# Kernel tuning notes

Hardware: AMD Instinct MI355X
Metric: run time of the kernel (lower is better)

Reference implementation:

```python
import jax, jax.numpy as jnp
import numpy as np

B, T, F = 4096, 512, 17
H = 32          # hidden_dim
P = 8           # num_prototypes
DEMO = 4
OUT = 1
FP = F + 1      # features + static row
LN_EPS = 1e-5
COS_EPS = 1e-8


def setup_inputs() -> dict:
    key = jax.random.key(0)
    ks = jax.random.split(key, 20)
    s = lambda i, shape, scale=0.1: jax.random.normal(ks[i], shape, jnp.float32) * scale
    return {
        "x": jax.random.normal(ks[0], (B, T, F), jnp.float32),
        "static": jax.random.normal(ks[1], (B, DEMO), jnp.float32),
        # 17 per-feature GRUs (input_size=1), batched along leading F axis
        "W_ih": s(2, (F, 3 * H)),      # squeezed from [F,3H,1]
        "W_hh": s(3, (F, 3 * H, H)),
        "b_ih": s(4, (F, 3 * H)),
        "b_hh": s(5, (F, 3 * H)),
        "demo_W": s(6, (H, DEMO)),
        "demo_b": s(7, (H,)),
        "ln_w": jnp.ones((FP, H), jnp.float32),
        "ln_b": jnp.zeros((FP, H), jnp.float32),
        "prototypes": jax.random.uniform(ks[8], (P, FP, H), jnp.float32),
        "Wq": s(9, (H, P)), "bq": s(10, (H,)),
        "Wk": s(11, (P, FP)), "bk": s(12, (P,)),
        "Wv": s(13, (P, FP)), "bv": s(14, (P,)),
        "out_W": s(15, (OUT, H)), "out_b": s(16, (OUT,)),
    }


def _batched_gru(x, W_ih, W_hh, b_ih, b_hh):
    # x: [B,T,F] -> run F independent GRUs (input dim 1) in parallel. Returns [B,F,H].
    h0 = jnp.zeros((x.shape[0], F, H), x.dtype)

    def step(h, x_t):  # x_t: [B,F]
        ih = x_t[:, :, None] * W_ih[None] + b_ih[None]                 # [B,F,3H]
        hh = jnp.einsum('bfh,fgh->bfg', h, W_hh) + b_hh[None]          # [B,F,3H]
        r = jax.nn.sigmoid(ih[..., :H] + hh[..., :H])
        z = jax.nn.sigmoid(ih[..., H:2 * H] + hh[..., H:2 * H])
        n = jnp.tanh(ih[..., 2 * H:] + r * hh[..., 2 * H:])
        h_new = (1.0 - z) * n + z * h
        return h_new, None

    h_final, _ = jax.lax.scan(step, h0, jnp.transpose(x, (1, 0, 2)))
    return h_final  # [B,F,H]


def reference(x, static, W_ih, W_hh, b_ih, b_hh, demo_W, demo_b,
              ln_w, ln_b, prototypes, Wq, bq, Wk, bk, Wv, bv, out_W, out_b):
    h_t = _batched_gru(x, W_ih, W_hh, b_ih, b_hh)                      # [B,F,H]
    demo = (static @ demo_W.T + demo_b)[:, None, :]                    # [B,1,H]
    h_t = jnp.concatenate([h_t, demo], axis=1)                         # [B,FP,H]
    # LayerNorm over last two dims (FP,H)
    mu = jnp.mean(h_t, axis=(-2, -1), keepdims=True)
    var = jnp.var(h_t, axis=(-2, -1), keepdims=True)
    h_t = (h_t - mu) * jax.lax.rsqrt(var + LN_EPS) * ln_w + ln_b
    # cosine similarity to flattened prototypes -> [B,P]
    hf = h_t.reshape(h_t.shape[0], -1)                                 # [B,FP*H]
    pf = prototypes.reshape(P, -1)                                     # [P,FP*H]
    num = hf @ pf.T
    denom = jnp.maximum(jnp.linalg.norm(hf, axis=-1)[:, None] *
                        jnp.linalg.norm(pf, axis=-1)[None, :], COS_EPS)
    distance = num / denom                                             # [B,P]
    # Attention1 (dropout inactive at eval)
    q = distance @ Wq.T + bq                                           # [B,H]
    input_k = jnp.einsum('bfh,pf->bph', h_t, Wk) + bk[None, :, None]   # [B,P,H]
    input_v = jnp.einsum('bfh,pf->bph', h_t, Wv) + bv[None, :, None]   # [B,P,H]
    e = jnp.einsum('bph,bh->bp', input_k, q)                           # [B,P]
    a = jax.nn.softmax(e, axis=1)
    v = jnp.einsum('bp,bph->bh', a, input_v)                           # [B,H]
    logits = jax.nn.sigmoid(v @ out_W.T + out_b)                       # [B,1]
    return logits, distance, h_t
```

## Files before the change

### kernel.cpp

```cpp
#include <hip/hip_runtime.h>
#include <cmath>

#define Bsz  4096
#define Tlen 512
#define Fnum 17
#define Hdim 32
#define Pnum 8
#define FPn  18
#define G3   96

#define L2E   1.4426950408889634f
#define NL2E (-1.4426950408889634f)
#define TL2E  2.8853900817779268f

typedef __attribute__((ext_vector_type(8))) short short8v;
typedef __attribute__((ext_vector_type(4))) float float4v;

__device__ __forceinline__ float frcp(float x)  { return __builtin_amdgcn_rcpf(x); }
__device__ __forceinline__ float frsq(float x)  { return __builtin_amdgcn_rsqf(x); }
__device__ __forceinline__ float fexp2(float x) { return __builtin_amdgcn_exp2f(x); }
__device__ __forceinline__ float fsigmoid(float x) {
    return frcp(1.0f + fexp2(NL2E * x));
}
__device__ __forceinline__ short bf16b(float x) {
    unsigned u = __float_as_uint(x);
    unsigned r = (u + 0x7FFFu + ((u >> 16) & 1u)) >> 16;
    return (short)r;
}
__device__ __forceinline__ unsigned cvtpk(float lo, float hi) {
    unsigned r;
    asm("v_cvt_pk_bf16_f32 %0, %1, %2" : "=v"(r) : "v"(lo), "v"(hi));
    return r;
}

__global__ void prep_pnorm_kernel(const float* __restrict__ protos, float* __restrict__ pnorm) {
    const int p    = threadIdx.x >> 5;
    const int lane = threadIdx.x & 31;
    float s = 0.0f;
    for (int j = lane; j < FPn * Hdim; j += 32) {
        float v = protos[p * FPn * Hdim + j];
        s = fmaf(v, v, s);
    }
    #pragma unroll
    for (int m = 16; m; m >>= 1) s += __shfl_xor(s, m);
    if (lane == 0) pnorm[p] = sqrtf(s);
}

__global__ __launch_bounds__(64)
void xpose_kernel(const float* __restrict__ x, unsigned short* __restrict__ xT) {
    const int b = blockIdx.x * 64 + threadIdx.x;
    const int t = blockIdx.y;
    const float* __restrict__ xp = x + ((size_t)b * Tlen + t) * Fnum;
    #pragma unroll
    for (int ff = 0; ff < Fnum; ++ff)
        xT[(size_t)ff * (Tlen + 1) * Bsz + (size_t)t * Bsz + b] = (unsigned short)bf16b(xp[ff]);
}

template<int USE_XT>
__global__ __launch_bounds__(256, 4)
void gru_mfma_kernel(const float* __restrict__ x,
                     const unsigned short* __restrict__ xT,
                     const float* __restrict__ Wih,
                     const float* __restrict__ Whh,
                     const float* __restrict__ bih,
                     const float* __restrict__ bhh,
                     float* __restrict__ pre)
{
    const int f  = blockIdx.y;
    const int wv = threadIdx.x >> 6;
    const int l  = threadIdx.x & 63;
    const int B0 = blockIdx.x * 64 + wv * 16;
    const int c  = l & 15, S = l >> 4;
    const int b  = B0 + c;

    const float* __restrict__ whh_f = Whh + (size_t)f * G3 * Hdim;
    const float* __restrict__ wih_f = Wih + (size_t)f * G3;
    const float* __restrict__ bih_f = bih + (size_t)f * G3;
    const float* __restrict__ bhh_f = bhh + (size_t)f * G3;

    short8v afrag0, afrag1, afrag2, afrag3, afrag4, afrag5;
    float4v cinit0, cinit1, cinit2, cinit3, cinit4, cinit5;
    {
        union { short8v s; unsigned u[4]; } au;
        #pragma unroll
        for (int m = 0; m < 6; ++m) {
            const int gate = m >> 1;
            const float sc = (gate < 2) ? NL2E : TL2E;
            const int gA = gate * 32 + 8 * (c >> 2) + (m & 1) * 4 + (c & 3);
            const float* wrow = whh_f + (size_t)gA * Hdim + 8 * S;
            #pragma unroll
            for (int u = 0; u < 4; ++u)
                au.u[u] = cvtpk(wrow[2 * u] * sc, wrow[2 * u + 1] * sc);
            float4v ci;
            #pragma unroll
            for (int q = 0; q < 4; ++q) {
                const int gC = gate * 32 + 8 * S + (m & 1) * 4 + q;
                ci[q] = (gate < 2) ? NL2E * (bhh_f[gC] + bih_f[gC])
                                   : TL2E * bhh_f[gC];
            }
            if (m == 0) { afrag0 = au.s; cinit0 = ci; }
            if (m == 1) { afrag1 = au.s; cinit1 = ci; }
            if (m == 2) { afrag2 = au.s; cinit2 = ci; }
            if (m == 3) { afrag3 = au.s; cinit3 = ci; }
            if (m == 4) { afrag4 = au.s; cinit4 = ci; }
            if (m == 5) { afrag5 = au.s; cinit5 = ci; }
        }
    }
    float wr[8], wz[8], wn[8], bn[8];
    #pragma unroll
    for (int i = 0; i < 8; ++i) {
        const int j = 8 * S + i;
        wr[i] = NL2E * wih_f[j];
        wz[i] = NL2E * wih_f[32 + j];
        wn[i] = TL2E * wih_f[64 + j];
        bn[i] = TL2E * bih_f[64 + j];
    }

    float h[8];
    #pragma unroll
    for (int i = 0; i < 8; ++i) h[i] = 0.0f;

    const unsigned short* xtp = nullptr;
    const float* xp = nullptr;
    float xv_next;
    if (USE_XT) {
        xtp = xT + (size_t)f * (Tlen + 1) * Bsz + b;
        xv_next = __uint_as_float(((unsigned)*xtp) << 16);
    } else {
        xp = x + (size_t)b * Tlen * Fnum + f;
        xv_next = *xp;
    }

    for (int t = 0; t < Tlen; ++t) {
        const float xv = xv_next;
        if (USE_XT) {
            xtp += Bsz;
            xv_next = __uint_as_float(((unsigned)*xtp) << 16);
        } else {
            xp += (t < Tlen - 1) ? Fnum : 0;
            xv_next = *xp;
        }

        union { short8v s; unsigned u[4]; } bu;
        bu.u[0] = cvtpk(h[0], h[1]);
        bu.u[1] = cvtpk(h[2], h[3]);
        bu.u[2] = cvtpk(h[4], h[5]);
        bu.u[3] = cvtpk(h[6], h[7]);

        const float4v a0 = __builtin_amdgcn_mfma_f32_16x16x32_bf16(afrag0, bu.s, cinit0, 0, 0, 0);
        const float4v a1 = __builtin_amdgcn_mfma_f32_16x16x32_bf16(afrag1, bu.s, cinit1, 0, 0, 0);
        const float4v a2 = __builtin_amdgcn_mfma_f32_16x16x32_bf16(afrag2, bu.s, cinit2, 0, 0, 0);
        const float4v a3 = __builtin_amdgcn_mfma_f32_16x16x32_bf16(afrag3, bu.s, cinit3, 0, 0, 0);
        const float4v a4 = __builtin_amdgcn_mfma_f32_16x16x32_bf16(afrag4, bu.s, cinit4, 0, 0, 0);
        const float4v a5 = __builtin_amdgcn_mfma_f32_16x16x32_bf16(afrag5, bu.s, cinit5, 0, 0, 0);

        #pragma unroll
        for (int i = 0; i < 8; ++i) {
            const int q = i & 3;
            const float ar = (i < 4) ? a0[q] : a1[q];
            const float az = (i < 4) ? a2[q] : a3[q];
            const float an = (i < 4) ? a4[q] : a5[q];

            const float er = fexp2(fmaf(xv, wr[i], ar));
            const float r  = frcp(1.0f + er);
            const float ez = fexp2(fmaf(xv, wz[i], az));
            const float E  = fexp2(fmaf(r, an, fmaf(xv, wn[i], bn[i])));
            const float num = fmaf(ez, E, -ez) + fmaf(h[i], E, h[i]);
            const float den = (E + 1.0f) * (1.0f + ez);
            h[i] = num * frcp(den);
        }
    }

    float* __restrict__ o = pre + (size_t)b * (FPn * Hdim) + f * Hdim + 8 * S;
    #pragma unroll
    for (int i = 0; i < 8; ++i) o[i] = h[i];
}

__global__ __launch_bounds__(256)
void post_kernel(const float* __restrict__ pre,
                 const float* __restrict__ statics,
                 const float* __restrict__ demoW,
                 const float* __restrict__ demob,
                 const float* __restrict__ lnw,
                 const float* __restrict__ lnb,
                 const float* __restrict__ protos,
                 const float* __restrict__ pnorm,
                 const float* __restrict__ Wq,
                 const float* __restrict__ bq,
                 const float* __restrict__ Wk,
                 const float* __restrict__ bk,
                 const float* __restrict__ Wv,
                 const float* __restrict__ bv,
                 const float* __restrict__ outW,
                 const float* __restrict__ outb,
                 float* __restrict__ out_logits,
                 float* __restrict__ out_dist,
                 float* __restrict__ out_ht)
{
    const int b     = blockIdx.x * 4 + (threadIdx.x >> 6);
    const int l     = threadIdx.x & 63;
    const int hl    = l & 31;
    const int fbase = (l >> 5) * 9;

    float v[9];
    #pragma unroll
    for (int j = 0; j < 9; ++j) {
        const int fj = fbase + j;
        if (fj == 17) {
            float acc = demob[hl];
            #pragma unroll
            for (int d = 0; d < 4; ++d)
                acc = fmaf(statics[b * 4 + d], demoW[hl * 4 + d], acc);
            v[j] = acc;
        } else {
            v[j] = pre[(size_t)b * 576 + fj * 32 + hl];
        }
    }

    float s = 0.0f, ss = 0.0f;
    #pragma unroll
    for (int j = 0; j < 9; ++j) { s += v[j]; ss = fmaf(v[j], v[j], ss); }
    #pragma unroll
    for (int m = 32; m; m >>= 1) { s += __shfl_xor(s, m); ss += __shfl_xor(ss, m); }
    const float mu  = s * (1.0f / 576.0f);
    const float var = ss * (1.0f / 576.0f) - mu * mu;
    const float rs  = frsq(var + 1e-5f);

    float nrm = 0.0f;
    #pragma unroll
    for (int j = 0; j < 9; ++j) {
        const int fj = fbase + j;
        float y = fmaf((v[j] - mu) * rs, lnw[fj * 32 + hl], lnb[fj * 32 + hl]);
        v[j] = y;
        out_ht[(size_t)b * 576 + fj * 32 + hl] = y;
        nrm = fmaf(y, y, nrm);
    }
    #pragma unroll
    for (int m = 32; m; m >>= 1) nrm += __shfl_xor(nrm, m);
    nrm = sqrtf(nrm);

    float dist[8];
    #pragma unroll
    for (int p = 0; p < Pnum; ++p) {
        float d = 0.0f;
        #pragma unroll
        for (int j = 0; j < 9; ++j)
            d = fmaf(v[j], protos[p * 576 + (fbase + j) * 32 + hl], d);
        #pragma unroll
        for (int m = 32; m; m >>= 1) d += __shfl_xor(d, m);
        dist[p] = d / fmaxf(nrm * pnorm[p], 1e-8f);
    }
    if (l == 0) {
        #pragma unroll
        for (int p = 0; p < Pnum; ++p) out_dist[(size_t)b * Pnum + p] = dist[p];
    }

    float q = bq[hl];
    #pragma unroll
    for (int p = 0; p < Pnum; ++p) q = fmaf(dist[p], Wq[hl * 8 + p], q);
    float Sq = q;
    #pragma unroll
    for (int m = 16; m; m >>= 1) Sq += __shfl_xor(Sq, m);

    float sf[9], so[9];
    #pragma unroll
    for (int j = 0; j < 9; ++j) {
        float t = v[j] * q;
        #pragma unroll
        for (int m = 16; m; m >>= 1) t += __shfl_xor(t, m);
        sf[j] = t;
    }
    #pragma unroll
    for (int j = 0; j < 9; ++j) so[j] = __shfl_xor(sf[j], 32);
    const int obase = 9 - fbase;

    float e[8];
    #pragma unroll
    for (int p = 0; p < Pnum; ++p) {
        float a = bk[p] * Sq;
        #pragma unroll
        for (int j = 0; j < 9; ++j) {
            a = fmaf(sf[j], Wk[p * FPn + fbase + j], a);
            a = fmaf(so[j], Wk[p * FPn + obase + j], a);
        }
        e[p] = a;
    }
    float mx = e[0];
    #pragma unroll
    for (int p = 1; p < Pnum; ++p) mx = fmaxf(mx, e[p]);
    float aw[8], den = 0.0f;
    #pragma unroll
    for (int p = 0; p < Pnum; ++p) { aw[p] = __expf(e[p] - mx); den += aw[p]; }
    const float rden = frcp(den);
    #pragma unroll
    for (int p = 0; p < Pnum; ++p) aw[p] *= rden;

    float cc = 0.0f;
    #pragma unroll
    for (int p = 0; p < Pnum; ++p) cc = fmaf(aw[p], bv[p], cc);
    float vb = 0.0f;
    #pragma unroll
    for (int j = 0; j < 9; ++j) {
        float wv = 0.0f;
        #pragma unroll
        for (int p = 0; p < Pnum; ++p) wv = fmaf(aw[p], Wv[p * FPn + fbase + j], wv);
        vb = fmaf(v[j], wv, vb);
    }
    vb += __shfl_xor(vb, 32);
    vb += cc;

    float lg = vb * outW[hl];
    #pragma unroll
    for (int m = 16; m; m >>= 1) lg += __shfl_xor(lg, m);
    lg = fsigmoid(lg + outb[0]);
    if (l == 0) out_logits[b] = lg;
}

extern "C" void kernel_launch(void* const* d_in, const int* in_sizes, int n_in,
                              void* d_out, int out_size, void* d_ws, size_t ws_size,
                              hipStream_t stream) {
    const float* x      = (const float*)d_in[0];
    const float* statics= (const float*)d_in[1];
    const float* Wih    = (const float*)d_in[2];
    const float* Whh    = (const float*)d_in[3];
    const float* bih    = (const float*)d_in[4];
    const float* bhh    = (const float*)d_in[5];
    const float* demoW  = (const float*)d_in[6];
    const float* demob  = (const float*)d_in[7];
    const float* lnw    = (const float*)d_in[8];
    const float* lnb    = (const float*)d_in[9];
    const float* protos = (const float*)d_in[10];
    const float* Wq     = (const float*)d_in[11];
    const float* bq     = (const float*)d_in[12];
    const float* Wk     = (const float*)d_in[13];
    const float* bk     = (const float*)d_in[14];
    const float* Wv     = (const float*)d_in[15];
    const float* bv     = (const float*)d_in[16];
    const float* outW   = (const float*)d_in[17];
    const float* outb   = (const float*)d_in[18];

    float* pre   = (float*)d_ws;
    float* pnorm = pre + (size_t)Bsz * FPn * Hdim;
    unsigned short* xT = (unsigned short*)(pnorm + 8);
    const size_t need = ((size_t)Bsz * FPn * Hdim + 8) * 4
                      + (size_t)Fnum * (Tlen + 1) * Bsz * 2;
    const bool use_xt = (ws_size >= need);

    prep_pnorm_kernel<<<dim3(1), dim3(256), 0, stream>>>(protos, pnorm);

    if (use_xt) {
        xpose_kernel<<<dim3(Bsz / 64, Tlen), dim3(64), 0, stream>>>(x, xT);
        gru_mfma_kernel<1><<<dim3(Bsz / 64, Fnum), dim3(256), 0, stream>>>(
            x, xT, Wih, Whh, bih, bhh, pre);
    } else {
        gru_mfma_kernel<0><<<dim3(Bsz / 64, Fnum), dim3(256), 0, stream>>>(
            x, xT, Wih, Whh, bih, bhh, pre);
    }

    float* out_logits = (float*)d_out;
    float* out_dist   = out_logits + Bsz;
    float* out_ht     = out_dist + (size_t)Bsz * Pnum;

    post_kernel<<<dim3(Bsz / 4), dim3(256), 0, stream>>>(
        pre, statics, demoW, demob, lnw, lnb, protos, pnorm,
        Wq, bq, Wk, bk, Wv, bv, outW, outb,
        out_logits, out_dist, out_ht);
}
```

Before: 965.6 us.

## Fold GRU input projection into MFMA and pack gate math into float2 pairs

Moves the per-step x*W_ih input terms out of scalar FMAs and into a second chained MFMA per gate tile, using a weight fragment that holds W_ih in one K column and an x operand held only by the S==0 lanes. Gate nonlinearities are rewritten with float2 vectors so paired FMAs can be emitted, and the time loop is manually unrolled by four with a rolling prefetch of x. The aim is fewer VALU instructions on the serial recurrence. In exchange it adds six extra MFMAs per step, which lengthens the dependent chain, and rounds x and W_ih to bf16 inside the MFMA.

Measured after the change: 845.8 us. -12.4%, faster.

```diff
diff --git a/kernel.cpp b/kernel.cpp
--- a/kernel.cpp
+++ b/kernel.cpp
@@ -8,6 +8,7 @@
 #define Pnum 8
 #define FPn  18
 #define G3   96
+#define TPAD 8
 
 #define L2E   1.4426950408889634f
 #define NL2E (-1.4426950408889634f)
@@ -15,12 +16,16 @@
 
 typedef __attribute__((ext_vector_type(8))) short short8v;
 typedef __attribute__((ext_vector_type(4))) float float4v;
+typedef __attribute__((ext_vector_type(2))) float float2v;
 
 __device__ __forceinline__ float frcp(float x)  { return __builtin_amdgcn_rcpf(x); }
 __device__ __forceinline__ float frsq(float x)  { return __builtin_amdgcn_rsqf(x); }
 __device__ __forceinline__ float fexp2(float x) { return __builtin_amdgcn_exp2f(x); }
 __device__ __forceinline__ float fsigmoid(float x) {
     return frcp(1.0f + fexp2(NL2E * x));
+}
+__device__ __forceinline__ float2v fma2(float2v a, float2v b, float2v c) {
+    return __builtin_elementwise_fma(a, b, c);
 }
 __device__ __forceinline__ short bf16b(float x) {
     unsigned u = __float_as_uint(x);
@@ -53,7 +58,7 @@
     const float* __restrict__ xp = x + ((size_t)b * Tlen + t) * Fnum;
     #pragma unroll
     for (int ff = 0; ff < Fnum; ++ff)
-        xT[(size_t)ff * (Tlen + 1) * Bsz + (size_t)t * Bsz + b] = (unsigned short)bf16b(xp[ff]);
+        xT[(size_t)ff * (Tlen + TPAD) * Bsz + (size_t)t * Bsz + b] = (unsigned short)bf16b(xp[ff]);
 }
 
 template<int USE_XT>
@@ -78,10 +83,13 @@
     const float* __restrict__ bih_f = bih + (size_t)f * G3;
     const float* __restrict__ bhh_f = bhh + (size_t)f * G3;
 
-    short8v afrag0, afrag1, afrag2, afrag3, afrag4, afrag5;
-    float4v cinit0, cinit1, cinit2, cinit3, cinit4, cinit5;
+    short8v af0, af1, af2, af3, af4, af5;
+    short8v g0, g1, g2, g3, g4, g5;
+    float4v cin0, cin1, cin2, cin3, cin4, cin5;
+    float4v cb4, cb5;
+    const float4v zero4 = {0.0f, 0.0f, 0.0f, 0.0f};
     {
-        union { short8v s; unsigned u[4]; } au;
+        union { short8v s; unsigned u[4]; } au, gu;
         #pragma unroll
         for (int m = 0; m < 6; ++m) {
             const int gate = m >> 1;
@@ -91,6 +99,8 @@
             #pragma unroll
             for (int u = 0; u < 4; ++u)
                 au.u[u] = cvtpk(wrow[2 * u] * sc, wrow[2 * u + 1] * sc);
+            gu.u[0] = (S == 0) ? cvtpk(sc * wih_f[gA], 0.0f) : 0u;
+            gu.u[1] = 0u; gu.u[2] = 0u; gu.u[3] = 0u;
             float4v ci;
             #pragma unroll
             for (int q = 0; q < 4; ++q) {
@@ -98,82 +108,101 @@
                 ci[q] = (gate < 2) ? NL2E * (bhh_f[gC] + bih_f[gC])
                                    : TL2E * bhh_f[gC];
             }
-            if (m == 0) { afrag0 = au.s; cinit0 = ci; }
-            if (m == 1) { afrag1 = au.s; cinit1 = ci; }
-            if (m == 2) { afrag2 = au.s; cinit2 = ci; }
-            if (m == 3) { afrag3 = au.s; cinit3 = ci; }
-            if (m == 4) { afrag4 = au.s; cinit4 = ci; }
-            if (m == 5) { afrag5 = au.s; cinit5 = ci; }
+            if (m == 0) { af0 = au.s; g0 = gu.s; cin0 = ci; }
+            if (m == 1) { af1 = au.s; g1 = gu.s; cin1 = ci; }
+            if (m == 2) { af2 = au.s; g2 = gu.s; cin2 = ci; }
+            if (m == 3) { af3 = au.s; g3 = gu.s; cin3 = ci; }
+            if (m == 4) { af4 = au.s; g4 = gu.s; cin4 = ci; }
+            if (m == 5) { af5 = au.s; g5 = gu.s; cin5 = ci; }
         }
-    }
-    float wr[8], wz[8], wn[8], bn[8];
-    #pragma unroll
-    for (int i = 0; i < 8; ++i) {
-        const int j = 8 * S + i;
-        wr[i] = NL2E * wih_f[j];
-        wz[i] = NL2E * wih_f[32 + j];
-        wn[i] = TL2E * wih_f[64 + j];
-        bn[i] = TL2E * bih_f[64 + j];
-    }
-
-    float h[8];
-    #pragma unroll
-    for (int i = 0; i < 8; ++i) h[i] = 0.0f;
-
-    const unsigned short* xtp = nullptr;
-    const float* xp = nullptr;
-    float xv_next;
+        #pragma unroll
+        for (int q = 0; q < 4; ++q) {
+            cb4[q] = TL2E * bih_f[64 + 8 * S + q];
+            cb5[q] = TL2E * bih_f[64 + 8 * S + 4 + q];
+        }
+    }
+    const float sm = (S == 0) ? 1.0f : 0.0f;
+
+    float2v h0 = {0,0}, h1 = {0,0}, h2 = {0,0}, h3 = {0,0};
+
+    const unsigned short* xtp = USE_XT ? (xT + (size_t)f * (Tlen + TPAD) * Bsz + b) : nullptr;
+    const float* xp = USE_XT ? nullptr : (x + (size_t)b * Tlen * Fnum + f);
+    float x0, x1, x2, x3;
     if (USE_XT) {
-        xtp = xT + (size_t)f * (Tlen + 1) * Bsz + b;
-        xv_next = __uint_as_float(((unsigned)*xtp) << 16);
+        x0 = __uint_as_float(((unsigned)xtp[0 * Bsz]) << 16);
+        x1 = __uint_as_float(((unsigned)xtp[1 * Bsz]) << 16);
+        x2 = __uint_as_float(((unsigned)xtp[2 * Bsz]) << 16);
+        x3 = __uint_as_float(((unsigned)xtp[3 * Bsz]) << 16);
     } else {
-        xp = x + (size_t)b * Tlen * Fnum + f;
-        xv_next = *xp;
-    }
-
-    for (int t = 0; t < Tlen; ++t) {
-        const float xv = xv_next;
-        if (USE_XT) {
-            xtp += Bsz;
-            xv_next = __uint_as_float(((unsigned)*xtp) << 16);
-        } else {
-            xp += (t < Tlen - 1) ? Fnum : 0;
-            xv_next = *xp;
-        }
-
-        union { short8v s; unsigned u[4]; } bu;
-        bu.u[0] = cvtpk(h[0], h[1]);
-        bu.u[1] = cvtpk(h[2], h[3]);
-        bu.u[2] = cvtpk(h[4], h[5]);
-        bu.u[3] = cvtpk(h[6], h[7]);
-
-        const float4v a0 = __builtin_amdgcn_mfma_f32_16x16x32_bf16(afrag0, bu.s, cinit0, 0, 0, 0);
-        const float4v a1 = __builtin_amdgcn_mfma_f32_16x16x32_bf16(afrag1, bu.s, cinit1, 0, 0, 0);
-        const float4v a2 = __builtin_amdgcn_mfma_f32_16x16x32_bf16(afrag2, bu.s, cinit2, 0, 0, 0);
-        const float4v a3 = __builtin_amdgcn_mfma_f32_16x16x32_bf16(afrag3, bu.s, cinit3, 0, 0, 0);
-        const float4v a4 = __builtin_amdgcn_mfma_f32_16x16x32_bf16(afrag4, bu.s, cinit4, 0, 0, 0);
-        const float4v a5 = __builtin_amdgcn_mfma_f32_16x16x32_bf16(afrag5, bu.s, cinit5, 0, 0, 0);
-
-        #pragma unroll
-        for (int i = 0; i < 8; ++i) {
-            const int q = i & 3;
-            const float ar = (i < 4) ? a0[q] : a1[q];
-            const float az = (i < 4) ? a2[q] : a3[q];
-            const float an = (i < 4) ? a4[q] : a5[q];
-
-            const float er = fexp2(fmaf(xv, wr[i], ar));
-            const float r  = frcp(1.0f + er);
-            const float ez = fexp2(fmaf(xv, wz[i], az));
-            const float E  = fexp2(fmaf(r, an, fmaf(xv, wn[i], bn[i])));
-            const float num = fmaf(ez, E, -ez) + fmaf(h[i], E, h[i]);
-            const float den = (E + 1.0f) * (1.0f + ez);
-            h[i] = num * frcp(den);
-        }
+        x0 = xp[0 * Fnum]; x1 = xp[1 * Fnum]; x2 = xp[2 * Fnum]; x3 = xp[3 * Fnum];
+    }
+
+#define LOADX(ph) (USE_XT ? __uint_as_float(((unsigned)xtp[(size_t)(ph) * Bsz]) << 16) \
+                          : ((t + (ph) < Tlen) ? xp[(size_t)(ph) * Fnum] : 0.0f))
+
+#define GATE_PAIR(hp, ar, az, an, en)                                           \
+    {                                                                           \
+        const float2v _ar = (ar), _az = (az), _an = (an), _en = (en);           \
+        float2v er = {fexp2(_ar.x), fexp2(_ar.y)};                              \
+        float2v rp = er + (float2v){1.0f, 1.0f};                                \
+        float2v r  = {frcp(rp.x), frcp(rp.y)};                                  \
+        float2v ez = {fexp2(_az.x), fexp2(_az.y)};                              \
+        float2v y  = fma2(r, _an, _en);                                         \
+        float2v E  = {fexp2(y.x), fexp2(y.y)};                                  \
+        float2v num = fma2(ez, E, -ez) + fma2(hp, E, hp);                       \
+        float2v den = (E + (float2v){1.0f, 1.0f}) * (ez + (float2v){1.0f, 1.0f});\
+        float2v rd = {frcp(den.x), frcp(den.y)};                                \
+        hp = num * rd;                                                          \
+    }
+
+#define LO2(v) ((float2v){(v)[0], (v)[1]})
+#define HI2(v) ((float2v){(v)[2], (v)[3]})
+
+#define GRU_STEP(xv)                                                            \
+    {                                                                           \
+        union { short8v s; unsigned u[4]; } bu;                                 \
+        bu.u[0] = cvtpk(h0.x, h0.y);                                            \
+        bu.u[1] = cvtpk(h1.x, h1.y);                                            \
+        bu.u[2] = cvtpk(h2.x, h2.y);                                            \
+        bu.u[3] = cvtpk(h3.x, h3.y);                                            \
+        union { short8v s; unsigned u[4]; } b2;                                 \
+        b2.u[0] = cvtpk((xv) * sm, 0.0f);                                       \
+        b2.u[1] = 0u; b2.u[2] = 0u; b2.u[3] = 0u;                               \
+        const float4v a0 = __builtin_amdgcn_mfma_f32_16x16x32_bf16(af0, bu.s, cin0, 0, 0, 0); \
+        const float4v a1 = __builtin_amdgcn_mfma_f32_16x16x32_bf16(af1, bu.s, cin1, 0, 0, 0); \
+        const float4v a2 = __builtin_amdgcn_mfma_f32_16x16x32_bf16(af2, bu.s, cin2, 0, 0, 0); \
+        const float4v a3 = __builtin_amdgcn_mfma_f32_16x16x32_bf16(af3, bu.s, cin3, 0, 0, 0); \
+        const float4v a4 = __builtin_amdgcn_mfma_f32_16x16x32_bf16(af4, bu.s, cin4, 0, 0, 0); \
+        const float4v a5 = __builtin_amdgcn_mfma_f32_16x16x32_bf16(af5, bu.s, cin5, 0, 0, 0); \
+        const float4v e0 = __builtin_amdgcn_mfma_f32_16x16x32_bf16(g0, b2.s, a0, 0, 0, 0); \
+        const float4v e1 = __builtin_amdgcn_mfma_f32_16x16x32_bf16(g1, b2.s, a1, 0, 0, 0); \
+        const float4v e2 = __builtin_amdgcn_mfma_f32_16x16x32_bf16(g2, b2.s, a2, 0, 0, 0); \
+        const float4v e3 = __builtin_amdgcn_mfma_f32_16x16x32_bf16(g3, b2.s, a3, 0, 0, 0); \
+        const float4v e4 = __builtin_amdgcn_mfma_f32_16x16x32_bf16(g4, b2.s, cb4, 0, 0, 0); \
+        const float4v e5 = __builtin_amdgcn_mfma_f32_16x16x32_bf16(g5, b2.s, cb5, 0, 0, 0); \
+        GATE_PAIR(h0, LO2(e0), LO2(e2), LO2(a4), LO2(e4));                      \
+        GATE_PAIR(h1, HI2(e0), HI2(e2), HI2(a4), HI2(e4));                      \
+        GATE_PAIR(h2, LO2(e1), LO2(e3), LO2(a5), LO2(e5));                      \
+        GATE_PAIR(h3, HI2(e1), HI2(e3), HI2(a5), HI2(e5));                      \
+    }
+
+    #pragma unroll 1
+    for (int t = 0; t < Tlen; t += 4) {
+        GRU_STEP(x0); x0 = LOADX(4);
+        GRU_STEP(x1); x1 = LOADX(5);
+        GRU_STEP(x2); x2 = LOADX(6);
+        GRU_STEP(x3); x3 = LOADX(7);
+        if (USE_XT) xtp += 4 * Bsz; else xp += 4 * Fnum;
     }
 
     float* __restrict__ o = pre + (size_t)b * (FPn * Hdim) + f * Hdim + 8 * S;
-    #pragma unroll
-    for (int i = 0; i < 8; ++i) o[i] = h[i];
+    o[0] = h0.x; o[1] = h0.y; o[2] = h1.x; o[3] = h1.y;
+    o[4] = h2.x; o[5] = h2.y; o[6] = h3.x; o[7] = h3.y;
+#undef GRU_STEP
+#undef GATE_PAIR
+#undef LOADX
+#undef LO2
+#undef HI2
 }
 
 __global__ __launch_bounds__(256)
@@ -343,7 +372,7 @@
     float* pnorm = pre + (size_t)Bsz * FPn * Hdim;
     unsigned short* xT = (unsigned short*)(pnorm + 8);
     const size_t need = ((size_t)Bsz * FPn * Hdim + 8) * 4
-                      + (size_t)Fnum * (Tlen + 1) * Bsz * 2;
+                      + (size_t)Fnum * (Tlen + TPAD) * Bsz * 2;
     const bool use_xt = (ws_size >= need);
 
     prep_pnorm_kernel<<<dim3(1), dim3(256), 0, stream>>>(protos, pnorm);
```
